# Performance work log

Hardware: AMD Instinct MI355X
Metric: run time of the kernel (lower is better)

The kernel has to match this reference:

```python
import jax, jax.numpy as jnp
import numpy as np

H = 2048          # hidden_size
NH = 32           # num_attention_heads
NKV = 8           # num_key_value_heads
HD = H // NH      # head_dim = 64
GROUPS = NH // NKV
B, S = 1, 4096


def setup_inputs() -> dict:
    key = jax.random.key(0)
    k1, k2, k3, k4, k5 = jax.random.split(key, 5)
    hidden_states = jax.random.normal(k1, (B, S, H), dtype=jnp.float32)
    # additive causal mask [B, 1, S, S]
    causal = jnp.tril(jnp.ones((S, S), dtype=bool))
    attention_mask = jnp.where(causal, 0.0, jnp.finfo(jnp.float32).min)[None, None].astype(jnp.float32)
    scale = 0.02
    Wq = jax.random.normal(k2, (H, H), dtype=jnp.float32) * scale
    Wk = jax.random.normal(k3, (NKV * HD, H), dtype=jnp.float32) * scale
    Wv = jax.random.normal(k4, (NKV * HD, H), dtype=jnp.float32) * scale
    Wo = jax.random.normal(k5, (H, H), dtype=jnp.float32) * scale
    return {"hidden_states": hidden_states, "attention_mask": attention_mask,
            "Wq": Wq, "Wk": Wk, "Wv": Wv, "Wo": Wo}


def reference(hidden_states, attention_mask, Wq, Wk, Wv, Wo):
    bsz, q_len, _ = hidden_states.shape
    # projections (nn.Linear: x @ W.T)
    q = (hidden_states @ Wq.T).reshape(bsz, q_len, NH, HD).transpose(0, 2, 1, 3)   # [B,NH,S,HD]
    k = (hidden_states @ Wk.T).reshape(bsz, q_len, NKV, HD).transpose(0, 2, 1, 3)  # [B,NKV,S,HD]
    v = (hidden_states @ Wv.T).reshape(bsz, q_len, NKV, HD).transpose(0, 2, 1, 3)
    # repeat_kv: expand each KV head GROUPS times
    k = jnp.repeat(k, GROUPS, axis=1)  # [B,NH,S,HD]
    v = jnp.repeat(v, GROUPS, axis=1)
    attn_weights = jnp.einsum('bhqd,bhkd->bhqk', q, k) / jnp.sqrt(jnp.float32(HD))
    attn_weights = attn_weights + attention_mask
    attn_weights = jax.nn.softmax(attn_weights.astype(jnp.float32), axis=-1).astype(q.dtype)
    attn_output = jnp.einsum('bhqk,bhkd->bhqd', attn_weights, v)
    attn_output = attn_output.transpose(0, 2, 1, 3).reshape(bsz, q_len, H)
    return attn_output @ Wo.T
```

## Files before the change

kernel.cpp:

```cpp
#include <hip/hip_runtime.h>
#include <stdint.h>

#define S_LEN  4096
#define HDIM   2048
#define NHEADS 32
#define NKVH   8
#define HDSZ   64
#define KVDIM  (NKVH * HDSZ)
#define QKN    (HDIM + KVDIM)

typedef __bf16 v8bf16 __attribute__((ext_vector_type(8)));
typedef short  v4s    __attribute__((ext_vector_type(4)));
typedef float  v4f32  __attribute__((ext_vector_type(4)));

__device__ __forceinline__ unsigned short f2bf(float f) {
    uint32_t u = __builtin_bit_cast(uint32_t, f);
    uint32_t r = (u + 0x7fffu + ((u >> 16) & 1u)) >> 16;
    return (unsigned short)r;
}

__device__ __forceinline__ uint32_t pack_bf16(float a, float b) {
#if __has_builtin(__builtin_amdgcn_cvt_pk_bf16_f32)
    auto r = __builtin_amdgcn_cvt_pk_bf16_f32(a, b);
    return __builtin_bit_cast(uint32_t, r);
#else
    uint32_t ua = __builtin_bit_cast(uint32_t, a) + 0x8000u;
    uint32_t ub = __builtin_bit_cast(uint32_t, b) + 0x8000u;
    return (ua >> 16) | (ub & 0xffff0000u);
#endif
}

__device__ __forceinline__ float fast_exp2(float x) {
#if __has_builtin(__builtin_amdgcn_exp2f)
    return __builtin_amdgcn_exp2f(x);
#else
    float r; asm("v_exp_f32 %0, %1" : "=v"(r) : "v"(x)); return r;
#endif
}

__device__ __forceinline__ void async_load16(const void* g, void* l) {
    __builtin_amdgcn_global_load_lds((const __attribute__((address_space(1))) void*)g,
                                     (__attribute__((address_space(3))) void*)l,
                                     16, 0, 0);
}

#define SEG0 2097152
#define SEG1 3145728
#define SEG2 3407872
#define SEG3 3670016
#define SEGT 4718592
__global__ void cvt_all(const float* __restrict__ x,  const float* __restrict__ wq,
                        const float* __restrict__ wk, const float* __restrict__ wv,
                        const float* __restrict__ wo,
                        ushort4* __restrict__ xb, ushort4* __restrict__ wqkb,
                        ushort4* __restrict__ wvb, ushort4* __restrict__ wob,
                        float qscale)
{
    int i = blockIdx.x * blockDim.x + threadIdx.x;
    if (i >= SEGT) return;
    const float4* src; ushort4* dst; float s = 1.0f; int loc;
    if (i < SEG0)      { src = (const float4*)x;  dst = xb;   loc = i; }
    else if (i < SEG1) { src = (const float4*)wq; dst = wqkb; loc = i - SEG0; s = qscale; }
    else if (i < SEG2) { src = (const float4*)wk; dst = wqkb + 1048576; loc = i - SEG1; }
    else if (i < SEG3) { src = (const float4*)wv; dst = wvb;  loc = i - SEG2; }
    else               { src = (const float4*)wo; dst = wob;  loc = i - SEG3; }
    float4 f = src[loc];
    uint2 o;
    o.x = pack_bf16(f.x * s, f.y * s);
    o.y = pack_bf16(f.z * s, f.w * s);
    dst[loc] = __builtin_bit_cast(ushort4, o);
}

__device__ __forceinline__ void gemm_tile_body(
    const unsigned short* __restrict__ A, const unsigned short* __restrict__ B,
    unsigned short* __restrict__ C, int N, int K, int m0, int n0,
    unsigned short* As, unsigned short* Bs)
{
    const int tid  = threadIdx.x;
    const int wave = tid >> 6;
    const int lane = tid & 63;
    const int lrow = lane & 15;
    const int quad = lane >> 4;
    const int wm = (wave >> 1) * 64;
    const int wn = (wave & 1) * 64;

    const int srow = wave * 32 + (lane >> 3);
    const int sg   = (lane & 7) ^ ((lane >> 3) & 7);
    const size_t aOff = (size_t)(m0 + srow) * K + sg * 8;
    const size_t bOff = (size_t)(n0 + srow) * K + sg * 8;

    v4f32 acc[4][4];
#pragma unroll
    for (int mi = 0; mi < 4; ++mi)
#pragma unroll
        for (int ni = 0; ni < 4; ++ni)
#pragma unroll
            for (int r = 0; r < 4; ++r) acc[mi][ni][r] = 0.0f;

    for (int k0 = 0; k0 < K; k0 += 64) {
#pragma unroll
        for (int i = 0; i < 4; ++i) {
            async_load16(A + aOff + (size_t)(i * 8) * K + k0,
                         &As[(wave * 32 + i * 8) * 64]);
            async_load16(B + bOff + (size_t)(i * 8) * K + k0,
                         &Bs[(wave * 32 + i * 8) * 64]);
        }
        __syncthreads();
#pragma unroll
        for (int ks = 0; ks < 2; ++ks) {
            const int kg  = ks * 4 + quad;
            const int swz = (kg ^ (lrow & 7)) * 8;
            v8bf16 af[4], bfm[4];
#pragma unroll
            for (int mi = 0; mi < 4; ++mi)
                af[mi] = *(const v8bf16*)&As[(wm + mi * 16 + lrow) * 64 + swz];
#pragma unroll
            for (int ni = 0; ni < 4; ++ni)
                bfm[ni] = *(const v8bf16*)&Bs[(wn + ni * 16 + lrow) * 64 + swz];
#pragma unroll
            for (int mi = 0; mi < 4; ++mi)
#pragma unroll
                for (int ni = 0; ni < 4; ++ni)
                    acc[mi][ni] = __builtin_amdgcn_mfma_f32_16x16x32_bf16(
                        af[mi], bfm[ni], acc[mi][ni], 0, 0, 0);
        }
        __syncthreads();
    }

#pragma unroll
    for (int mi = 0; mi < 4; ++mi)
#pragma unroll
        for (int ni = 0; ni < 4; ++ni)
#pragma unroll
            for (int r = 0; r < 4; ++r) {
                const int row = m0 + wm + mi * 16 + quad * 4 + r;
                const int col = n0 + wn + ni * 16 + lrow;
                C[(size_t)row * N + col] = f2bf(acc[mi][ni][r]);
            }
}

__global__ __launch_bounds__(256)
void gemm_qkv(const unsigned short* __restrict__ xb,
              const unsigned short* __restrict__ Wqkb,
              const unsigned short* __restrict__ Wvb,
              unsigned short* __restrict__ QKb,
              unsigned short* __restrict__ Vtb)
{
    __shared__ unsigned short As[128 * 64];
    __shared__ unsigned short Bs[128 * 64];
    const int bid = blockIdx.x;
    if (bid < 128) {
        gemm_tile_body(Wvb, xb, Vtb, S_LEN, HDIM,
                       (bid & 3) * 128, (bid >> 2) * 128, As, Bs);
    } else {
        const int b = bid - 128;
        gemm_tile_body(xb, Wqkb, QKb, QKN, HDIM,
                       (b & 31) * 128, (b >> 5) * 128, As, Bs);
    }
}

__global__ __launch_bounds__(256)
void gemm_bt_f32(const unsigned short* __restrict__ A,
                 const unsigned short* __restrict__ B,
                 float* __restrict__ Cout, int M, int N, int K)
{
    __shared__ unsigned short As[128 * 64];
    __shared__ unsigned short Bs[128 * 64];

    const int tid  = threadIdx.x;
    const int wave = tid >> 6;
    const int lane = tid & 63;
    const int lrow = lane & 15;
    const int quad = lane >> 4;

    const int m0 = blockIdx.x * 128;
    const int n0 = blockIdx.y * 128;
    const int wm = (wave >> 1) * 64;
    const int wn = (wave & 1) * 64;

    const int srow = wave * 32 + (lane >> 3);
    const int sg   = (lane & 7) ^ ((lane >> 3) & 7);
    const size_t aOff = (size_t)(m0 + srow) * K + sg * 8;
    const size_t bOff = (size_t)(n0 + srow) * K + sg * 8;

    v4f32 acc[4][4];
#pragma unroll
    for (int mi = 0; mi < 4; ++mi)
#pragma unroll
        for (int ni = 0; ni < 4; ++ni)
#pragma unroll
            for (int r = 0; r < 4; ++r) acc[mi][ni][r] = 0.0f;

    for (int k0 = 0; k0 < K; k0 += 64) {
#pragma unroll
        for (int i = 0; i < 4; ++i) {
            async_load16(A + aOff + (size_t)(i * 8) * K + k0,
                         &As[(wave * 32 + i * 8) * 64]);
            async_load16(B + bOff + (size_t)(i * 8) * K + k0,
                         &Bs[(wave * 32 + i * 8) * 64]);
        }
        __syncthreads();
#pragma unroll
        for (int ks = 0; ks < 2; ++ks) {
            const int kg  = ks * 4 + quad;
            const int swz = (kg ^ (lrow & 7)) * 8;
            v8bf16 af[4], bfm[4];
#pragma unroll
            for (int mi = 0; mi < 4; ++mi)
                af[mi] = *(const v8bf16*)&As[(wm + mi * 16 + lrow) * 64 + swz];
#pragma unroll
            for (int ni = 0; ni < 4; ++ni)
                bfm[ni] = *(const v8bf16*)&Bs[(wn + ni * 16 + lrow) * 64 + swz];
#pragma unroll
            for (int mi = 0; mi < 4; ++mi)
#pragma unroll
                for (int ni = 0; ni < 4; ++ni)
                    acc[mi][ni] = __builtin_amdgcn_mfma_f32_16x16x32_bf16(
                        af[mi], bfm[ni], acc[mi][ni], 0, 0, 0);
        }
        __syncthreads();
    }

#pragma unroll
    for (int mi = 0; mi < 4; ++mi)
#pragma unroll
        for (int ni = 0; ni < 4; ++ni)
#pragma unroll
            for (int r = 0; r < 4; ++r) {
                const int row = m0 + wm + mi * 16 + quad * 4 + r;
                const int col = n0 + wn + ni * 16 + lrow;
                Cout[(size_t)row * N + col] = acc[mi][ni][r];
            }
}

__global__ __launch_bounds__(256, 4)
void flash_attn(const unsigned short* __restrict__ QK,
                const unsigned short* __restrict__ Vt,
                unsigned short* __restrict__ O)
{
    __shared__ unsigned short smem[24576];
    unsigned short* Qs  = smem;
    unsigned short* KsB = smem + 8192;
    unsigned short* VsB = smem + 16384;

    const int tid  = threadIdx.x;
    const int wave = tid >> 6;
    const int lane = tid & 63;
    const int lrow = lane & 15;
    const int quad = lane >> 4;

    const int h   = blockIdx.x;
    const int kvh = h >> 2;
    const int q0  = (gridDim.y - 1 - blockIdx.y) * 128;

    const int srow8 = lane >> 3;
    const int sgrp  = (lane & 7) ^ srow8;
    const v4s v_one = {0x3F80, 0x3F80, 0x3F80, 0x3F80};

    auto stageKV = [&](int k0, int sel) {
        unsigned short* Ks = KsB + sel * 4096;
        unsigned short* Vs = VsB + sel * 4096;
        const size_t gk = (size_t)(k0 + wave * 16 + srow8) * QKN
                          + HDIM + kvh * HDSZ + sgrp * 8;
        async_load16(QK + gk,             &Ks[(wave * 16) * 64]);
        async_load16(QK + gk + 8 * QKN,   &Ks[(wave * 16 + 8) * 64]);
        const size_t gv = (size_t)(kvh * HDSZ + wave * 16 + srow8) * S_LEN
                          + k0 + sgrp * 8;
        async_load16(Vt + gv,             &Vs[(wave * 16) * 64]);
        async_load16(Vt + gv + 8 * S_LEN, &Vs[(wave * 16 + 8) * 64]);
    };

    {
        const size_t gq = (size_t)(q0 + wave * 32 + srow8) * QKN + h * HDSZ + sgrp * 8;
#pragma unroll
        for (int i = 0; i < 4; ++i)
            async_load16(QK + gq + (size_t)(i * 8) * QKN, &Qs[(wave * 32 + i * 8) * 64]);
    }
    stageKV(0, 0);

    v4f32 o_acc[2][4], l_acc[2];
#pragma unroll
    for (int mi = 0; mi < 2; ++mi) {
#pragma unroll
        for (int r = 0; r < 4; ++r) l_acc[mi][r] = 0.0f;
#pragma unroll
        for (int dj = 0; dj < 4; ++dj)
#pragma unroll
            for (int r = 0; r < 4; ++r) o_acc[mi][dj][r] = 0.0f;
    }

    const int rbase = q0 + wave * 32;
    const int njt   = (q0 >> 6) + 2;

    for (int j = 0; j < njt; ++j) {
        const int k0  = j * 64;
        const int cur = j & 1;
        asm volatile("s_waitcnt vmcnt(0)" ::: "memory");
        asm volatile("s_barrier" ::: "memory");
        if (j + 1 < njt) stageKV((j + 1) * 64, 1 - cur);

        if (k0 > rbase + 31) continue;

        const unsigned short* Ks = KsB + cur * 4096;
        const unsigned short* Vs = VsB + cur * 4096;

        v4f32 st[2][4];
#pragma unroll
        for (int mi = 0; mi < 2; ++mi)
#pragma unroll
            for (int nj = 0; nj < 4; ++nj)
#pragma unroll
                for (int r = 0; r < 4; ++r) st[mi][nj][r] = 0.0f;
#pragma unroll
        for (int kk = 0; kk < 2; ++kk) {
            const int swz = ((kk * 4 + quad) ^ (lrow & 7)) * 8;
            v8bf16 qa[2];
            qa[0] = *(const v8bf16*)&Qs[(wave * 32 + lrow) * 64 + swz];
            qa[1] = *(const v8bf16*)&Qs[(wave * 32 + 16 + lrow) * 64 + swz];
#pragma unroll
            for (int nj = 0; nj < 4; ++nj) {
                const v8bf16 kb = *(const v8bf16*)&Ks[(nj * 16 + lrow) * 64 + swz];
                st[0][nj] = __builtin_amdgcn_mfma_f32_16x16x32_bf16(kb, qa[0], st[0][nj], 0, 0, 0);
                st[1][nj] = __builtin_amdgcn_mfma_f32_16x16x32_bf16(kb, qa[1], st[1][nj], 0, 0, 0);
            }
        }

        if (k0 + 63 > rbase) {
#pragma unroll
            for (int mi = 0; mi < 2; ++mi) {
                const int qi = rbase + mi * 16 + lrow;
#pragma unroll
                for (int nj = 0; nj < 4; ++nj) {
                    const int kib = k0 + nj * 16 + quad * 4;
#pragma unroll
                    for (int r = 0; r < 4; ++r)
                        if (kib + r > qi) st[mi][nj][r] = -1e30f;
                }
            }
        }

        v4s pk[2][4];
#pragma unroll
        for (int mi = 0; mi < 2; ++mi)
#pragma unroll
            for (int nj = 0; nj < 4; ++nj) {
                const float p0 = fast_exp2(st[mi][nj][0]);
                const float p1 = fast_exp2(st[mi][nj][1]);
                const float p2 = fast_exp2(st[mi][nj][2]);
                const float p3 = fast_exp2(st[mi][nj][3]);
                uint2 u;
                u.x = pack_bf16(p0, p1);
                u.y = pack_bf16(p2, p3);
                pk[mi][nj] = __builtin_bit_cast(v4s, u);
            }

#pragma unroll
        for (int t = 0; t < 4; ++t) {
            v4s va[4];
#pragma unroll
            for (int dj = 0; dj < 4; ++dj)
                va[dj] = *(const v4s*)&Vs[(dj * 16 + lrow) * 64 +
                                          (((t * 2 + (quad >> 1)) ^ (lrow & 7)) * 8) + (quad & 1) * 4];
#pragma unroll
            for (int dj = 0; dj < 4; ++dj) {
                o_acc[0][dj] = __builtin_amdgcn_mfma_f32_16x16x16bf16_1k(va[dj], pk[0][t], o_acc[0][dj], 0, 0, 0);
                o_acc[1][dj] = __builtin_amdgcn_mfma_f32_16x16x16bf16_1k(va[dj], pk[1][t], o_acc[1][dj], 0, 0, 0);
            }
            l_acc[0] = __builtin_amdgcn_mfma_f32_16x16x16bf16_1k(v_one, pk[0][t], l_acc[0], 0, 0, 0);
            l_acc[1] = __builtin_amdgcn_mfma_f32_16x16x16bf16_1k(v_one, pk[1][t], l_acc[1], 0, 0, 0);
        }
    }

    __syncthreads();
    unsigned short* Os = smem;
#pragma unroll
    for (int mi = 0; mi < 2; ++mi) {
        const float inv = 1.0f / l_acc[mi][0];
#pragma unroll
        for (int dj = 0; dj < 4; ++dj)
#pragma unroll
            for (int r = 0; r < 4; ++r)
                Os[(wave * 32 + mi * 16 + lrow) * 72 + dj * 16 + quad * 4 + r] =
                    f2bf(o_acc[mi][dj][r] * inv);
    }
    __syncthreads();
#pragma unroll
    for (int i = 0; i < 4; ++i) {
        const int idx = i * 256 + tid;
        const int row = idx >> 3, c8 = idx & 7;
        const uint4 vv = *(const uint4*)&Os[row * 72 + c8 * 8];
        *(uint4*)&O[(size_t)(q0 + row) * HDIM + h * HDSZ + c8 * 8] = vv;
    }
}

extern "C" void kernel_launch(void* const* d_in, const int* in_sizes, int n_in,
                              void* d_out, int out_size, void* d_ws, size_t ws_size,
                              hipStream_t stream)
{
    const float* x  = (const float*)d_in[0];
    const float* Wq = (const float*)d_in[2];
    const float* Wk = (const float*)d_in[3];
    const float* Wv = (const float*)d_in[4];
    const float* Wo = (const float*)d_in[5];
    float* out = (float*)d_out;

    unsigned short* xb   = (unsigned short*)d_ws;
    unsigned short* Wqkb = xb   + (size_t)S_LEN * HDIM;
    unsigned short* Wvb  = Wqkb + (size_t)QKN * HDIM;
    unsigned short* Wob  = Wvb  + (size_t)KVDIM * HDIM;
    unsigned short* QKb  = Wob  + (size_t)HDIM * HDIM;
    unsigned short* Vtb  = QKb  + (size_t)S_LEN * QKN;
    unsigned short* AOb  = xb;

    cvt_all<<<(SEGT + 255) / 256, 256, 0, stream>>>(
        x, Wq, Wk, Wv, Wo,
        (ushort4*)xb, (ushort4*)Wqkb, (ushort4*)Wvb, (ushort4*)Wob,
        0.18033688011f);

    gemm_qkv<<<768, 256, 0, stream>>>(xb, Wqkb, Wvb, QKb, Vtb);

    flash_attn<<<dim3(NHEADS, S_LEN / 128), 256, 0, stream>>>(QKb, Vtb, AOb);

    gemm_bt_f32<<<dim3(S_LEN / 128, HDIM / 128), 256, 0, stream>>>(
        AOb, Wob, out, S_LEN, HDIM, HDIM);
}
```

Measured before the change: 372.9 us.

## Use 16x16x32 MFMA for PV via permuted K rows, drop KV double buffering

Loads the K rows in a permuted order so that each lane's packed P values line up with the 32-wide K dimension of the bf16 16x16x32 MFMA. The PV product and the row-sum product then issue half as many, wider MFMA instructions and read V with 16-byte LDS loads. The causal mask indices are remapped to match the permutation. The KV tile loses its double buffer: shared memory shrinks from 48KB to 32KB, and every tile is loaded synchronously between two barriers, so load latency is no longer overlapped with compute.

New measurement: 340.4 us. 8.7% less time.

```diff
diff --git a/kernel.cpp b/kernel.cpp
--- a/kernel.cpp
+++ b/kernel.cpp
@@ -238,10 +238,10 @@
                 const unsigned short* __restrict__ Vt,
                 unsigned short* __restrict__ O)
 {
-    __shared__ unsigned short smem[24576];
-    unsigned short* Qs  = smem;
-    unsigned short* KsB = smem + 8192;
-    unsigned short* VsB = smem + 16384;
+    __shared__ unsigned short smem[16384];
+    unsigned short* Qs = smem;
+    unsigned short* Ks = smem + 128 * 64;
+    unsigned short* Vs = smem + 128 * 64 + 64 * 64;
 
     const int tid  = threadIdx.x;
     const int wave = tid >> 6;
@@ -255,20 +255,8 @@
 
     const int srow8 = lane >> 3;
     const int sgrp  = (lane & 7) ^ srow8;
-    const v4s v_one = {0x3F80, 0x3F80, 0x3F80, 0x3F80};
-
-    auto stageKV = [&](int k0, int sel) {
-        unsigned short* Ks = KsB + sel * 4096;
-        unsigned short* Vs = VsB + sel * 4096;
-        const size_t gk = (size_t)(k0 + wave * 16 + srow8) * QKN
-                          + HDIM + kvh * HDSZ + sgrp * 8;
-        async_load16(QK + gk,             &Ks[(wave * 16) * 64]);
-        async_load16(QK + gk + 8 * QKN,   &Ks[(wave * 16 + 8) * 64]);
-        const size_t gv = (size_t)(kvh * HDSZ + wave * 16 + srow8) * S_LEN
-                          + k0 + sgrp * 8;
-        async_load16(Vt + gv,             &Vs[(wave * 16) * 64]);
-        async_load16(Vt + gv + 8 * S_LEN, &Vs[(wave * 16 + 8) * 64]);
-    };
+    const v8bf16 v_one8 = __builtin_bit_cast(v8bf16,
+        (uint4){0x3F803F80u, 0x3F803F80u, 0x3F803F80u, 0x3F803F80u});
 
     {
         const size_t gq = (size_t)(q0 + wave * 32 + srow8) * QKN + h * HDSZ + sgrp * 8;
@@ -276,7 +264,14 @@
         for (int i = 0; i < 4; ++i)
             async_load16(QK + gq + (size_t)(i * 8) * QKN, &Qs[(wave * 32 + i * 8) * 64]);
     }
-    stageKV(0, 0);
+
+    int kperm[2];
+#pragma unroll
+    for (int i = 0; i < 2; ++i) {
+        const int slot = wave * 16 + i * 8 + srow8;
+        const int nj = slot >> 4, sm = slot & 15;
+        kperm[i] = 32 * (nj >> 1) + 8 * (sm >> 2) + 4 * (nj & 1) + (sm & 3);
+    }
 
     v4f32 o_acc[2][4], l_acc[2];
 #pragma unroll
@@ -293,16 +288,23 @@
     const int njt   = (q0 >> 6) + 2;
 
     for (int j = 0; j < njt; ++j) {
-        const int k0  = j * 64;
-        const int cur = j & 1;
-        asm volatile("s_waitcnt vmcnt(0)" ::: "memory");
-        asm volatile("s_barrier" ::: "memory");
-        if (j + 1 < njt) stageKV((j + 1) * 64, 1 - cur);
+        const int k0 = j * 64;
+        __syncthreads();
+        {
+#pragma unroll
+            for (int i = 0; i < 2; ++i) {
+                const size_t gk = (size_t)(k0 + kperm[i]) * QKN
+                                  + HDIM + kvh * HDSZ + sgrp * 8;
+                async_load16(QK + gk, &Ks[(wave * 16 + i * 8) * 64]);
+            }
+            const size_t gv = (size_t)(kvh * HDSZ + wave * 16 + srow8) * S_LEN
+                              + k0 + sgrp * 8;
+            async_load16(Vt + gv,             &Vs[(wave * 16) * 64]);
+            async_load16(Vt + gv + 8 * S_LEN, &Vs[(wave * 16 + 8) * 64]);
+        }
+        __syncthreads();
 
         if (k0 > rbase + 31) continue;
-
-        const unsigned short* Ks = KsB + cur * 4096;
-        const unsigned short* Vs = VsB + cur * 4096;
 
         v4f32 st[2][4];
 #pragma unroll
@@ -331,7 +333,7 @@
                 const int qi = rbase + mi * 16 + lrow;
 #pragma unroll
                 for (int nj = 0; nj < 4; ++nj) {
-                    const int kib = k0 + nj * 16 + quad * 4;
+                    const int kib = k0 + 32 * (nj >> 1) + 8 * quad + 4 * (nj & 1);
 #pragma unroll
                     for (int r = 0; r < 4; ++r)
                         if (kib + r > qi) st[mi][nj][r] = -1e30f;
@@ -339,35 +341,37 @@
             }
         }
 
-        v4s pk[2][4];
-#pragma unroll
-        for (int mi = 0; mi < 2; ++mi)
+        v8bf16 pk8[2][2];
+#pragma unroll
+        for (int mi = 0; mi < 2; ++mi) {
+            uint2 pu[4];
 #pragma unroll
             for (int nj = 0; nj < 4; ++nj) {
                 const float p0 = fast_exp2(st[mi][nj][0]);
                 const float p1 = fast_exp2(st[mi][nj][1]);
                 const float p2 = fast_exp2(st[mi][nj][2]);
                 const float p3 = fast_exp2(st[mi][nj][3]);
-                uint2 u;
-                u.x = pack_bf16(p0, p1);
-                u.y = pack_bf16(p2, p3);
-                pk[mi][nj] = __builtin_bit_cast(v4s, u);
-            }
-
-#pragma unroll
-        for (int t = 0; t < 4; ++t) {
-            v4s va[4];
+                pu[nj].x = pack_bf16(p0, p1);
+                pu[nj].y = pack_bf16(p2, p3);
+            }
+            pk8[mi][0] = __builtin_bit_cast(v8bf16, (uint4){pu[0].x, pu[0].y, pu[1].x, pu[1].y});
+            pk8[mi][1] = __builtin_bit_cast(v8bf16, (uint4){pu[2].x, pu[2].y, pu[3].x, pu[3].y});
+        }
+
+#pragma unroll
+        for (int t = 0; t < 2; ++t) {
+            const int swzv = ((t * 4 + quad) ^ (lrow & 7)) * 8;
+            v8bf16 va[4];
 #pragma unroll
             for (int dj = 0; dj < 4; ++dj)
-                va[dj] = *(const v4s*)&Vs[(dj * 16 + lrow) * 64 +
-                                          (((t * 2 + (quad >> 1)) ^ (lrow & 7)) * 8) + (quad & 1) * 4];
+                va[dj] = *(const v8bf16*)&Vs[(dj * 16 + lrow) * 64 + swzv];
 #pragma unroll
             for (int dj = 0; dj < 4; ++dj) {
-                o_acc[0][dj] = __builtin_amdgcn_mfma_f32_16x16x16bf16_1k(va[dj], pk[0][t], o_acc[0][dj], 0, 0, 0);
-                o_acc[1][dj] = __builtin_amdgcn_mfma_f32_16x16x16bf16_1k(va[dj], pk[1][t], o_acc[1][dj], 0, 0, 0);
-            }
-            l_acc[0] = __builtin_amdgcn_mfma_f32_16x16x16bf16_1k(v_one, pk[0][t], l_acc[0], 0, 0, 0);
-            l_acc[1] = __builtin_amdgcn_mfma_f32_16x16x16bf16_1k(v_one, pk[1][t], l_acc[1], 0, 0, 0);
+                o_acc[0][dj] = __builtin_amdgcn_mfma_f32_16x16x32_bf16(va[dj], pk8[0][t], o_acc[0][dj], 0, 0, 0);
+                o_acc[1][dj] = __builtin_amdgcn_mfma_f32_16x16x32_bf16(va[dj], pk8[1][t], o_acc[1][dj], 0, 0, 0);
+            }
+            l_acc[0] = __builtin_amdgcn_mfma_f32_16x16x32_bf16(v_one8, pk8[0][t], l_acc[0], 0, 0, 0);
+            l_acc[1] = __builtin_amdgcn_mfma_f32_16x16x32_bf16(v_one8, pk8[1][t], l_acc[1], 0, 0, 0);
         }
     }
 
```
